# Kernel optimization log

Measured on AMD Instinct MI355X. Metric: run time of the kernel, lower is better.

## Reference

```python
import jax, jax.numpy as jnp
import numpy as np

NEG_SLOPE = 0.2

def _leaky(x):
    return jnp.where(x >= 0, x, NEG_SLOPE * x)

def _unigat(X, W, b, ae, av, pair_e, pair_v, num_v, num_e):
    # theta
    Xp = X @ W + b                                                    # [N, d]
    # v2e mean aggregation -> hyperedge features
    deg_e = jax.ops.segment_sum(jnp.ones(pair_e.shape, jnp.float32), pair_e, num_segments=num_e)
    Y = jax.ops.segment_sum(Xp[pair_v], pair_e, num_segments=num_e) / jnp.maximum(deg_e, 1.0)[:, None]  # [E, d]
    # GAT-style attention per incidence pair (edge term + node term), dropout=identity in eval
    s = _leaky((Y @ ae)[pair_e] + (Xp @ av)[pair_v])                  # [P]
    # segment softmax over edges incident to each node
    m = jax.ops.segment_max(s, pair_v, num_segments=num_v)
    ex = jnp.exp(s - m[pair_v])
    den = jax.ops.segment_sum(ex, pair_v, num_segments=num_v)
    alpha = ex / den[pair_v]                                          # [P]
    out = jax.ops.segment_sum(alpha[:, None] * Y[pair_e], pair_v, num_segments=num_v)  # [N, d]
    return jax.nn.elu(out)  # is_last=False everywhere -> ELU (use_bn=False)

def _multi_head(X, W, b, ae, av, pair_e, pair_v, num_v, num_e):
    # W:[H,din,d] b:[H,d] ae/av:[H,d]; concat heads on feature dim
    f = lambda Wh, bh, aeh, avh: _unigat(X, Wh, bh, aeh, avh, pair_e, pair_v, num_v, num_e)
    outs = jax.vmap(f)(W, b, ae, av)                                  # [H, N, d]
    return jnp.transpose(outs, (1, 0, 2)).reshape(X.shape[0], -1)     # [N, H*d]

def setup_inputs() -> dict:
    key = jax.random.key(0)
    ks = jax.random.split(key, 12)
    N, E, P = 100000, 20000, 1600000
    din, dh, H, C = 128, 64, 4, 40
    concat = 2
    inp = {
        "x0": jax.random.normal(ks[0], (N, din), jnp.float32),
        "x1": jax.random.normal(ks[1], (N, din), jnp.float32),
        "W1": jax.random.normal(ks[2], (H, din, dh), jnp.float32) * 0.05,
        "b1": jnp.zeros((H, dh), jnp.float32),
        "ae1": jax.random.normal(ks[3], (H, dh), jnp.float32) * 0.05,
        "av1": jax.random.normal(ks[4], (H, dh), jnp.float32) * 0.05,
        "W2": jax.random.normal(ks[5], (concat * dh * H, C), jnp.float32) * 0.05,
        "b2": jnp.zeros((C,), jnp.float32),
        "ae2": jax.random.normal(ks[6], (C,), jnp.float32) * 0.05,
        "av2": jax.random.normal(ks[7], (C,), jnp.float32) * 0.05,
        "pair_e": jax.random.randint(ks[8], (P,), 0, E, jnp.int32),
        "pair_v": jax.random.randint(ks[9], (P,), 0, N, jnp.int32),
        "num_v": N,
        "num_e": E,
    }
    return inp

def reference(x0, x1, W1, b1, ae1, av1, W2, b2, ae2, av2, pair_e, pair_v, num_v, num_e):
    # dropout layers are identity in eval mode
    h0 = _multi_head(x0, W1, b1, ae1, av1, pair_e, pair_v, num_v, num_e)
    h1 = _multi_head(x1, W1, b1, ae1, av1, pair_e, pair_v, num_v, num_e)
    h = jnp.concatenate([h0, h1], axis=-1)                            # [N, concat*H*dh]
    return _unigat(h, W2, b2, ae2, av2, pair_e, pair_v, num_v, num_e) # [N, C]
```

## Files before the change

### kernel.cpp

```cpp
#include <hip/hip_runtime.h>
#include <cstdint>
#include <cstddef>

static constexpr int DIN = 128;
static constexpr int DH = 64;
static constexpr int NH = 4;
static constexpr int DCAT = 512;
static constexpr int NC = 40;
static constexpr int E_CONST = 20000;
static constexpr int SH_V = 9, SUBD_V = 512;
static constexpr int SH_E = 7, SUBD_E = 128;
static constexpr int ECH = 11, NSUB_E = 10;
static constexpr int VCH = 12, NSUB_V = 25;
static constexpr int CHUNKA = 4096;

typedef unsigned short u16;
typedef __attribute__((ext_vector_type(4))) unsigned short u16x4;
typedef __attribute__((ext_vector_type(8))) unsigned short u16x8;
typedef __attribute__((ext_vector_type(8))) short bf16x8;
typedef __attribute__((ext_vector_type(4))) float f32x4;

static __device__ __forceinline__ float bf2f(u16 u) {
    union { unsigned int i; float f; } x;
    x.i = ((unsigned int)u) << 16;
    return x.f;
}
static __device__ __forceinline__ u16 f2bf(float f) {
    union { float f; unsigned int i; } x;
    x.f = f;
    unsigned int r = x.i + 0x7fffu + ((x.i >> 16) & 1u);
    return (u16)(r >> 16);
}


__global__ void k_hist2(const int* __restrict__ pv, const int* __restrict__ pe,
                        int* __restrict__ btot_v, int* __restrict__ btot_e, int P) {
    __shared__ int cv[256], ce[256];
    int tid = threadIdx.x;
    cv[tid] = 0; ce[tid] = 0;
    __syncthreads();
    int p0 = blockIdx.x * CHUNKA;
    #pragma unroll
    for (int j = 0; j < CHUNKA / 256; ++j) {
        int p = p0 + tid + j * 256;
        if (p < P) {
            atomicAdd(&cv[pv[p] >> SH_V], 1);
            atomicAdd(&ce[pe[p] >> SH_E], 1);
        }
    }
    __syncthreads();
    if (cv[tid]) atomicAdd(&btot_v[tid], cv[tid]);
    if (ce[tid]) atomicAdd(&btot_e[tid], ce[tid]);
}

static __device__ void scan_body(int* a, int n) {
    __shared__ int wsum[16];
    __shared__ int carry_s;
    int tid = threadIdx.x;
    int lane = tid & 63;
    int w = tid >> 6;
    if (tid == 0) carry_s = 0;
    __syncthreads();
    for (int base = 0; base < n; base += 1024) {
        int i = base + tid;
        int v = (i < n) ? a[i] : 0;
        int x = v;
        #pragma unroll
        for (int off = 1; off < 64; off <<= 1) {
            int t = __shfl_up(x, off);
            if (lane >= off) x += t;
        }
        if (lane == 63) wsum[w] = x;
        __syncthreads();
        int woff = 0;
        for (int k = 0; k < w; ++k) woff += wsum[k];
        int carry = carry_s;
        if (i < n) a[i] = carry + woff + x - v;
        int tot = 0;
        for (int k = 0; k < 16; ++k) tot += wsum[k];
        __syncthreads();
        if (tid == 0) carry_s = carry + tot;
        __syncthreads();
    }
    if (tid == 0) a[n] = carry_s;
}

__global__ void k_scan_both(int* __restrict__ a, int na, int* __restrict__ b, int nb) {
    if (blockIdx.x == 0) scan_body(a, na);
    else scan_body(b, nb);
}

__global__ void k_scatter2way(const int* __restrict__ pv, const int* __restrict__ pe,
                              const int* __restrict__ bstart_v, const int* __restrict__ bstart_e,
                              int* __restrict__ cur_v, int* __restrict__ cur_e,
                              uint2* __restrict__ sorted_v, uint2* __restrict__ sorted_e, int P) {
    __shared__ int cv[256], ce[256], posv[256], pose[256];
    int tid = threadIdx.x;
    cv[tid] = 0; ce[tid] = 0;
    __syncthreads();
    int p0 = blockIdx.x * CHUNKA;
    int kv[CHUNKA / 256], ke[CHUNKA / 256];
    #pragma unroll
    for (int j = 0; j < CHUNKA / 256; ++j) {
        int p = p0 + tid + j * 256;
        if (p < P) {
            kv[j] = pv[p];
            ke[j] = pe[p];
            atomicAdd(&cv[kv[j] >> SH_V], 1);
            atomicAdd(&ce[ke[j] >> SH_E], 1);
        } else {
            kv[j] = -1;
            ke[j] = -1;
        }
    }
    __syncthreads();
    if (cv[tid]) posv[tid] = bstart_v[tid] + atomicAdd(&cur_v[tid], cv[tid]);
    if (ce[tid]) pose[tid] = bstart_e[tid] + atomicAdd(&cur_e[tid], ce[tid]);
    __syncthreads();
    #pragma unroll
    for (int j = 0; j < CHUNKA / 256; ++j) {
        if (kv[j] >= 0) {
            int iv = atomicAdd(&posv[kv[j] >> SH_V], 1);
            sorted_v[iv] = make_uint2((unsigned)kv[j], (unsigned)ke[j]);
            int ie = atomicAdd(&pose[ke[j] >> SH_E], 1);
            sorted_e[ie] = make_uint2((unsigned)ke[j], (unsigned)kv[j]);
        }
    }
}

template <int SUBD, int SH, int NSUB, int CSH>
__global__ __launch_bounds__(256) void k_build_ord(const uint2* __restrict__ sorted,
                                                   const int* __restrict__ bstart,
                                                   int* __restrict__ start_out,
                                                   int* __restrict__ deg_out,
                                                   int* __restrict__ csr_out, int D) {
    constexpr int NK2 = SUBD * NSUB;
    constexpr int STRIP = (NK2 + 255) / 256;
    __shared__ int cnt[NK2];
    __shared__ int wsum[4];
    int b = blockIdx.x;
    int tid = threadIdx.x;
    int base_key = b << SH;
    int s0 = bstart[b];
    int cntN = bstart[b + 1] - s0;
    for (int k = tid; k < NK2; k += 256) cnt[k] = 0;
    __syncthreads();
    for (int i = tid; i < cntN; i += 256) {
        uint2 pr = sorted[s0 + i];
        int k2 = ((int)pr.x - base_key) * NSUB + ((int)pr.y >> CSH);
        atomicAdd(&cnt[k2], 1);
    }
    __syncthreads();
    int local[STRIP];
    int sum = 0;
    int t0 = tid * STRIP;
    #pragma unroll
    for (int j = 0; j < STRIP; ++j) {
        int idx = t0 + j;
        local[j] = (idx < NK2) ? cnt[idx] : 0;
        sum += local[j];
    }
    int lane = tid & 63, w = tid >> 6;
    int x = sum;
    #pragma unroll
    for (int off = 1; off < 64; off <<= 1) {
        int t = __shfl_up(x, off);
        if (lane >= off) x += t;
    }
    if (lane == 63) wsum[w] = x;
    __syncthreads();
    int woff = 0;
    for (int k = 0; k < w; ++k) woff += wsum[k];
    int run = woff + x - sum;
    __syncthreads();
    #pragma unroll
    for (int j = 0; j < STRIP; ++j) {
        int idx = t0 + j;
        if (idx < NK2) {
            int tmp = local[j];
            cnt[idx] = run;
            run += tmp;
        }
    }
    __syncthreads();
    for (int loc = tid; loc < SUBD; loc += 256) {
        int key = base_key + loc;
        if (key < D) {
            int st = cnt[loc * NSUB];
            int en = (loc == SUBD - 1) ? cntN : cnt[(loc + 1) * NSUB];
            start_out[key] = s0 + st;
            deg_out[key] = en - st;
        }
    }
    __syncthreads();
    for (int i = tid; i < cntN; i += 256) {
        uint2 pr = sorted[s0 + i];
        int k2 = ((int)pr.x - base_key) * NSUB + ((int)pr.y >> CSH);
        int idx = atomicAdd(&cnt[k2], 1);
        csr_out[s0 + idx] = (int)pr.y;
    }
}

__global__ void k_prep(const float* __restrict__ W1, const float* __restrict__ b1,
                       const float* __restrict__ av1, const float* __restrict__ W2,
                       float* __restrict__ wav, float* __restrict__ bav,
                       u16* __restrict__ WcatT, u16* __restrict__ W2T) {
    int bid = blockIdx.x;
    int tid = threadIdx.x;
    if (bid < 4) {
        int h = bid;
        if (tid < DIN) {
            float s = 0.f;
            for (int j = 0; j < DH; ++j)
                s += W1[(size_t)(h * DIN + tid) * DH + j] * av1[h * DH + j];
            wav[h * DIN + tid] = s;
        }
        if (tid == 0) {
            float t = 0.f;
            for (int j = 0; j < DH; ++j) t += b1[h * DH + j] * av1[h * DH + j];
            bav[h] = t;
        }
    } else if (bid < 4 + 128) {
        int idx = (bid - 4) * 256 + tid;
        int c = idx >> 7, k = idx & 127;
        int h = c >> 6, j = c & 63;
        WcatT[c * DIN + k] = f2bf(W1[((size_t)h * DIN + k) * DH + j]);
    } else {
        int idx = (bid - 132) * 256 + tid;
        int c = idx >> 9, k = idx & 511;
        float v = (c < NC) ? W2[(size_t)k * NC + c] : 0.f;
        W2T[c * DCAT + k] = f2bf(v);
    }
}

__global__ void k_conv(const float* __restrict__ X0, const float* __restrict__ X1,
                       const float* __restrict__ wav, const float* __restrict__ bav,
                       u16* __restrict__ Xbi, float* __restrict__ sv8, int N) {
    int wave = (blockIdx.x * blockDim.x + threadIdx.x) >> 6;
    int lane = threadIdx.x & 63;
    if (wave >= N) return;
    int xz = blockIdx.y;
    const float* X = xz ? X1 : X0;
    float2 a = *(const float2*)(X + (size_t)wave * DIN + lane * 2);
    unsigned int packed = (unsigned int)f2bf(a.x) | ((unsigned int)f2bf(a.y) << 16);
    *(unsigned int*)(Xbi + (size_t)wave * 256 + xz * 128 + lane * 2) = packed;
    float s[NH];
    #pragma unroll
    for (int h = 0; h < NH; ++h) {
        float2 wv = *(const float2*)(wav + h * DIN + lane * 2);
        float t = a.x * wv.x + a.y * wv.y;
        #pragma unroll
        for (int off = 32; off >= 1; off >>= 1) t += __shfl_xor(t, off);
        s[h] = t;
    }
    if (lane == 0) {
        #pragma unroll
        for (int h = 0; h < NH; ++h) sv8[(size_t)(xz * 4 + h) * N + wave] = s[h] + bav[h];
    }
}

__global__ void k_edge_mean1(const u16* __restrict__ Xbi, const int* __restrict__ start_e,
                             const int* __restrict__ deg_e, const int* __restrict__ csr_e_v,
                             u16* __restrict__ Xbar0, u16* __restrict__ Xbar1, int E) {
    int wave = (blockIdx.x * blockDim.x + threadIdx.x) >> 6;
    int lane = threadIdx.x & 63;
    if (wave >= E) return;
    int s = start_e[wave], t = s + deg_e[wave];
    int q = lane >> 4, c = lane & 15;
    float a0[8], a1[8];
    #pragma unroll
    for (int j = 0; j < 8; ++j) { a0[j] = 0.f; a1[j] = 0.f; }
    int i = s + q;
    u16x8 y0A = {0}, y1A = {0}, y0B = {0}, y1B = {0}, y0C = {0}, y1C = {0};
#define EM1_LOAD(Y0, Y1, IDX) { int v_ = csr_e_v[IDX]; \
        const u16* yp_ = Xbi + (size_t)v_ * 256 + c * 8; \
        Y0 = *(const u16x8*)yp_; Y1 = *(const u16x8*)(yp_ + 128); }
#define EM1_CONSUME(Y0, Y1) { \
        _Pragma("unroll") \
        for (int j = 0; j < 8; ++j) { a0[j] += bf2f(Y0[j]); a1[j] += bf2f(Y1[j]); } }
    if (i < t) EM1_LOAD(y0A, y1A, i);
    if (i + 4 < t) EM1_LOAD(y0B, y1B, i + 4);
    if (i + 8 < t) EM1_LOAD(y0C, y1C, i + 8);
    for (; i + 8 < t; i += 12) {
        EM1_CONSUME(y0A, y1A);
        if (i + 12 < t) EM1_LOAD(y0A, y1A, i + 12);
        EM1_CONSUME(y0B, y1B);
        if (i + 16 < t) EM1_LOAD(y0B, y1B, i + 16);
        EM1_CONSUME(y0C, y1C);
        if (i + 20 < t) EM1_LOAD(y0C, y1C, i + 20);
    }
    if (i < t) EM1_CONSUME(y0A, y1A);
    if (i + 4 < t) EM1_CONSUME(y0B, y1B);
#undef EM1_LOAD
#undef EM1_CONSUME
    #pragma unroll
    for (int j = 0; j < 8; ++j) {
        a0[j] += __shfl_xor(a0[j], 16);
        a0[j] += __shfl_xor(a0[j], 32);
        a1[j] += __shfl_xor(a1[j], 16);
        a1[j] += __shfl_xor(a1[j], 32);
    }
    int deg = t - s;
    float inv = 1.f / (float)(deg > 1 ? deg : 1);
    if (q == 0) {
        u16x8 r0, r1;
        #pragma unroll
        for (int j = 0; j < 8; ++j) { r0[j] = f2bf(a0[j] * inv); r1[j] = f2bf(a1[j] * inv); }
        *(u16x8*)(Xbar0 + (size_t)wave * DIN + c * 8) = r0;
        *(u16x8*)(Xbar1 + (size_t)wave * DIN + c * 8) = r1;
    }
}

template <int KDIM, int NTILES, int DOTMODE>
__global__ __launch_bounds__(256) void k_gemm_mfma(const u16* __restrict__ A0,
                                                   const u16* __restrict__ A1, int M,
                                                   const u16* __restrict__ Bt,
                                                   const float* __restrict__ bias,
                                                   u16* __restrict__ out0, u16* __restrict__ out1,
                                                   int ldo, int ncols,
                                                   const float* __restrict__ dvec,
                                                   float* __restrict__ dout) {
    constexpr int LDB = KDIM + 8;
    __shared__ u16 Bs[NTILES * 16 * LDB];
    const u16* A = blockIdx.z ? A1 : A0;
    u16* out = blockIdx.z ? out1 : out0;
    int tid = threadIdx.x;
    int colbase = blockIdx.y * NTILES * 16;
    const u16* Btblk = Bt + (size_t)colbase * KDIM;
    for (int idx = tid * 4; idx < NTILES * 16 * KDIM; idx += 256 * 4) {
        int c = idx / KDIM, k = idx % KDIM;
        *(u16x4*)&Bs[c * LDB + k] = *(const u16x4*)(Btblk + c * KDIM + k);
    }
    __syncthreads();
    int w = tid >> 6, lane = tid & 63;
    int r0 = blockIdx.x * 64 + w * 16;
    int arow = r0 + (lane & 15);
    bool avalid = arow < M;
    const u16* ap = A + (size_t)arow * KDIM + (lane >> 4) * 8;
    f32x4 acc[NTILES];
    #pragma unroll
    for (int nt = 0; nt < NTILES; ++nt) acc[nt] = (f32x4){0.f, 0.f, 0.f, 0.f};
    #pragma unroll
    for (int k0 = 0; k0 < KDIM; k0 += 32) {
        bf16x8 a = (bf16x8)(short)0;
        if (avalid) a = *(const bf16x8*)(ap + k0);
        #pragma unroll
        for (int nt = 0; nt < NTILES; ++nt) {
            bf16x8 b = *(const bf16x8*)&Bs[(nt * 16 + (lane & 15)) * LDB + k0 + (lane >> 4) * 8];
            acc[nt] = __builtin_amdgcn_mfma_f32_16x16x32_bf16(a, b, acc[nt], 0, 0, 0);
        }
    }
    #pragma unroll
    for (int j = 0; j < 4; ++j) {
        int row = r0 + (lane >> 4) * 4 + j;
        float pA = 0.f, pB = 0.f;
        #pragma unroll
        for (int nt = 0; nt < NTILES; ++nt) {
            int col = colbase + nt * 16 + (lane & 15);
            bool cok = col < ncols;
            float val = cok ? acc[nt][j] + bias[col] : 0.f;
            if (DOTMODE == 1) {
                float dv = dvec[col];
                if (nt < NTILES / 2) pA += val * dv; else pB += val * dv;
            } else if (DOTMODE == 2) {
                pA += cok ? val * dvec[col] : 0.f;
            }
            if (row < M && cok) out[(size_t)row * ldo + col] = f2bf(val);
        }
        if (DOTMODE) {
            pA += __shfl_xor(pA, 1);
            pA += __shfl_xor(pA, 2);
            pA += __shfl_xor(pA, 4);
            pA += __shfl_xor(pA, 8);
            if (DOTMODE == 1) {
                pB += __shfl_xor(pB, 1);
                pB += __shfl_xor(pB, 2);
                pB += __shfl_xor(pB, 4);
                pB += __shfl_xor(pB, 8);
            }
            if ((lane & 15) == 0 && row < M) {
                if (DOTMODE == 1) {
                    int hbase = blockIdx.y * 2;
                    int z = blockIdx.z;
                    dout[(size_t)(z * 4 + hbase) * M + row] = pA;
                    dout[(size_t)(z * 4 + hbase + 1) * M + row] = pB;
                } else {
                    dout[row] = pA;
                }
            }
        }
    }
}

__global__ void k_node_pass1(const u16* __restrict__ Ycat, const float* __restrict__ se8,
                             const float* __restrict__ sv8, const int* __restrict__ start_v,
                             const int* __restrict__ deg_v, const int* __restrict__ csr_v_e,
                             u16* __restrict__ hbuf, int N, int E) {
    int bid = blockIdx.x;
    int s = bid & 7;
    int warp = threadIdx.x >> 6;
    int lane = threadIdx.x & 63;
    int g = lane >> 3, c = lane & 7;
    int node = (bid >> 3) * 32 + warp * 8 + g;
    if (node >= N) return;
    int p0 = start_v[node];
    int p1 = p0 + deg_v[node];
    float sv = sv8[(size_t)s * N + node];
    const float* seS = se8 + (size_t)s * E;
    const u16* ybase = Ycat + s * 64 + c * 8;
    float den = 0.f;
    float acc[8];
    #pragma unroll
    for (int j = 0; j < 8; ++j) acc[j] = 0.f;
    float sA = 0.f, sB = 0.f;
    u16x8 yA = {0}, yB = {0};
#define NP1_LOAD(S, Y, IDX) { int e_ = csr_v_e[IDX]; S = seS[e_]; \
        Y = *(const u16x8*)(ybase + (size_t)e_ * 512); }
#define NP1_CONSUME(S, Y) { \
        float x_ = S + sv; x_ = fmaxf(x_, 0.2f * x_); float ex_ = __expf(x_); \
        den += ex_; \
        _Pragma("unroll") \
        for (int j = 0; j < 8; ++j) acc[j] += ex_ * bf2f(Y[j]); }
    int i = p0;
    if (i < p1) NP1_LOAD(sA, yA, i);
    if (i + 1 < p1) NP1_LOAD(sB, yB, i + 1);
    for (; i + 1 < p1; i += 2) {
        NP1_CONSUME(sA, yA);
        if (i + 2 < p1) NP1_LOAD(sA, yA, i + 2);
        NP1_CONSUME(sB, yB);
        if (i + 3 < p1) NP1_LOAD(sB, yB, i + 3);
    }
    if (i < p1) NP1_CONSUME(sA, yA);
#undef NP1_LOAD
#undef NP1_CONSUME
    float inv = (p1 > p0) ? 1.f / den : 0.f;
    u16x8 r;
    #pragma unroll
    for (int j = 0; j < 8; ++j) {
        float o = acc[j] * inv;
        o = o > 0.f ? o : __expf(o) - 1.f;
        r[j] = f2bf(o);
    }
    *(u16x8*)(hbuf + (size_t)node * DCAT + s * 64 + c * 8) = r;
}


__global__ void k_edge_mean2(const u16* __restrict__ Xp2b, const int* __restrict__ start_e,
                             const int* __restrict__ deg_ea, const int* __restrict__ csr_e_v,
                             u16* __restrict__ Y2b, const float* __restrict__ ae2,
                             float* __restrict__ se2, int E) {
    int warp = threadIdx.x >> 6;
    int lane = threadIdx.x & 63;
    int g = lane >> 3, c = lane & 7;
    int edge = blockIdx.x * 32 + warp * 8 + g;
    if (edge >= E) return;
    int p0 = start_e[edge], p1 = p0 + deg_ea[edge];
    bool act = c < 5;
    const u16* xbase = Xp2b + c * 8;
    float acc[8];
    #pragma unroll
    for (int j = 0; j < 8; ++j) acc[j] = 0.f;
    if (act) {
        for (int i = p0; i < p1; ++i) {
            int v = csr_e_v[i];
            u16x8 y = *(const u16x8*)(xbase + (size_t)v * NC);
            #pragma unroll
            for (int j = 0; j < 8; ++j) acc[j] += bf2f(y[j]);
        }
    }
    int deg = p1 - p0;
    float inv = 1.f / (float)(deg > 1 ? deg : 1);
    float p = 0.f;
    if (act) {
        u16x8 r;
        #pragma unroll
        for (int j = 0; j < 8; ++j) {
            float y = acc[j] * inv;
            p += y * ae2[c * 8 + j];
            r[j] = f2bf(y);
        }
        *(u16x8*)(Y2b + (size_t)edge * NC + c * 8) = r;
    }
    p += __shfl_xor(p, 1);
    p += __shfl_xor(p, 2);
    p += __shfl_xor(p, 4);
    if (c == 0) se2[edge] = p;
}

__global__ void k_node_pass2(const u16* __restrict__ Y2b, const float* __restrict__ se2,
                             const float* __restrict__ sv2, const int* __restrict__ start_v,
                             const int* __restrict__ deg_va, const int* __restrict__ csr_v_e,
                             float* __restrict__ out, int N) {
    int warp = threadIdx.x >> 6;
    int lane = threadIdx.x & 63;
    int g = lane >> 3, c = lane & 7;
    int node = blockIdx.x * 32 + warp * 8 + g;
    if (node >= N) return;
    int p0 = start_v[node], p1 = p0 + deg_va[node];
    bool act = c < 5;
    float* orow = out + (size_t)node * NC;
    if (p1 == p0) {
        if (act) {
            *(float4*)(orow + c * 8) = make_float4(0.f, 0.f, 0.f, 0.f);
            *(float4*)(orow + c * 8 + 4) = make_float4(0.f, 0.f, 0.f, 0.f);
        }
        return;
    }
    float svv = sv2[node];
    const u16* ybase = Y2b + c * 8;
    float den = 0.f;
    float acc[8];
    #pragma unroll
    for (int j = 0; j < 8; ++j) acc[j] = 0.f;
    for (int i = p0; i < p1; ++i) {
        int e = csr_v_e[i];
        float x = se2[e] + svv;
        x = fmaxf(x, 0.2f * x);
        float ex = __expf(x);
        den += ex;
        if (act) {
            u16x8 y = *(const u16x8*)(ybase + (size_t)e * NC);
            #pragma unroll
            for (int j = 0; j < 8; ++j) acc[j] += ex * bf2f(y[j]);
        }
    }
    if (act) {
        float inv = 1.f / den;
        float o[8];
        #pragma unroll
        for (int j = 0; j < 8; ++j) {
            float v = acc[j] * inv;
            o[j] = v > 0.f ? v : __expf(v) - 1.f;
        }
        *(float4*)(orow + c * 8) = make_float4(o[0], o[1], o[2], o[3]);
        *(float4*)(orow + c * 8 + 4) = make_float4(o[4], o[5], o[6], o[7]);
    }
}

extern "C" void kernel_launch(void* const* d_in, const int* in_sizes, int n_in,
                              void* d_out, int out_size, void* d_ws, size_t ws_size,
                              hipStream_t stream) {
    const float* x0 = (const float*)d_in[0];
    const float* x1 = (const float*)d_in[1];
    const float* W1 = (const float*)d_in[2];
    const float* b1 = (const float*)d_in[3];
    const float* ae1 = (const float*)d_in[4];
    const float* av1 = (const float*)d_in[5];
    const float* W2 = (const float*)d_in[6];
    const float* b2 = (const float*)d_in[7];
    const float* ae2 = (const float*)d_in[8];
    const float* av2 = (const float*)d_in[9];
    const int* pe = (const int*)d_in[10];
    const int* pv = (const int*)d_in[11];

    const int N = in_sizes[0] / DIN;
    const int P = in_sizes[10];
    const int E = E_CONST;
    const int NBKT_V = (N + SUBD_V - 1) / SUBD_V;
    const int NBKT_E = (E + SUBD_E - 1) / SUBD_E;

    char* base = (char*)d_ws;
    auto alloc = [&](size_t bytes) -> void* {
        void* p = (void*)base;
        base += (bytes + 255) & ~(size_t)255;
        return p;
    };
    u16* Xbi = (u16*)alloc((size_t)N * 256 * 2);
    u16* hbuf = (u16*)alloc((size_t)N * DCAT * 2);
    u16* Xbar0 = (u16*)alloc((size_t)E * DIN * 2);
    u16* Xbar1 = (u16*)alloc((size_t)E * DIN * 2);
    u16* Ycat = (u16*)alloc((size_t)E * 512 * 2);
    u16* Xp2b = (u16*)alloc((size_t)N * NC * 2);
    u16* Y2b = (u16*)alloc((size_t)E * NC * 2);
    float* se8 = (float*)alloc((size_t)8 * E * 4);
    float* se2 = (float*)alloc((size_t)E * 4);
    float* sv8 = (float*)alloc((size_t)8 * N * 4);
    float* sv2 = (float*)alloc((size_t)N * 4);
    float* wav = (float*)alloc((size_t)NH * DIN * 4);
    float* bav = (float*)alloc((size_t)NH * 4);
    u16* WcatT = (u16*)alloc((size_t)256 * DIN * 2);
    u16* W2T = (u16*)alloc((size_t)48 * DCAT * 2);
    uint2* sorted_v = (uint2*)alloc((size_t)P * 8);
    uint2* sorted_e = (uint2*)alloc((size_t)P * 8);
    int* start_v = (int*)alloc((size_t)N * 4);
    int* deg_v = (int*)alloc((size_t)N * 4);
    int* start_e = (int*)alloc((size_t)E * 4);
    int* deg_e = (int*)alloc((size_t)E * 4);
    int* csr_v_e = (int*)alloc((size_t)P * 4);
    int* csr_e_v = (int*)alloc((size_t)P * 4);
    char* zstart = base;
    int* bstart_v = (int*)alloc((size_t)(NBKT_V + 1) * 4);
    int* bstart_e = (int*)alloc((size_t)(NBKT_E + 1) * 4);
    int* cur_v = (int*)alloc((size_t)256 * 4);
    int* cur_e = (int*)alloc((size_t)256 * 4);
    size_t zbytes = (size_t)(base - zstart);

    if ((size_t)(base - (char*)d_ws) > ws_size) return;

    hipMemsetAsync(zstart, 0, zbytes, stream);

    dim3 b256(256);
    int nA = (P + CHUNKA - 1) / CHUNKA;
    k_hist2<<<nA, b256, 0, stream>>>(pv, pe, bstart_v, bstart_e, P);
    k_scan_both<<<2, 1024, 0, stream>>>(bstart_v, NBKT_V, bstart_e, NBKT_E);
    k_scatter2way<<<nA, b256, 0, stream>>>(pv, pe, bstart_v, bstart_e, cur_v, cur_e,
                                           sorted_v, sorted_e, P);
    k_build_ord<SUBD_V, SH_V, NSUB_E, ECH><<<NBKT_V, b256, 0, stream>>>(sorted_v, bstart_v,
                                                                        start_v, deg_v,
                                                                        csr_v_e, N);
    k_build_ord<SUBD_E, SH_E, NSUB_V, VCH><<<NBKT_E, b256, 0, stream>>>(sorted_e, bstart_e,
                                                                        start_e, deg_e,
                                                                        csr_e_v, E);

    k_prep<<<228, b256, 0, stream>>>(W1, b1, av1, W2, wav, bav, WcatT, W2T);

    int gN4 = (N + 3) / 4;
    int gE4 = (E + 3) / 4;
    dim3 gconv(gN4, 2);
    k_conv<<<gconv, b256, 0, stream>>>(x0, x1, wav, bav, Xbi, sv8, N);

    k_edge_mean1<<<gE4, b256, 0, stream>>>(Xbi, start_e, deg_e, csr_e_v, Xbar0, Xbar1, E);
    dim3 g1((E + 63) / 64, 2, 2);
    k_gemm_mfma<DIN, 8, 1><<<g1, b256, 0, stream>>>(Xbar0, Xbar1, E, WcatT, b1,
                                                    Ycat, Ycat + 256, 512, 256, ae1, se8);
    int gnp1 = ((N + 31) / 32) * 8;
    k_node_pass1<<<gnp1, b256, 0, stream>>>(Ycat, se8, sv8, start_v, deg_v, csr_v_e,
                                            hbuf, N, E);

    dim3 g2((N + 63) / 64, 1, 1);
    k_gemm_mfma<DCAT, 3, 2><<<g2, b256, 0, stream>>>(hbuf, hbuf, N, W2T, b2, Xp2b, Xp2b,
                                                     NC, NC, av2, sv2);
    int gseg = (E + 31) / 32;
    k_edge_mean2<<<gseg, b256, 0, stream>>>(Xp2b, start_e, deg_e, csr_e_v, Y2b, ae2, se2, E);
    int gnp2 = (N + 31) / 32;
    k_node_pass2<<<gnp2, b256, 0, stream>>>(Y2b, se2, sv2, start_v, deg_v, csr_v_e,
                                            (float*)d_out, N);
}
```

Baseline: 600.5 us.

## Process nodes and edges in degree-sorted order to balance warp work

Adds a counting sort of nodes and hyperedges by degree that builds a permutation, and makes node_pass1, edge_mean2 and node_pass2 visit items in that order. The goal is that the eight groups within a warp see similar segment lengths, so fewer lanes sit idle waiting on the longest segment. In exchange it adds five small launches for the sort plus one extra indirection per item, and output writes become scattered rather than contiguous.

Result: slower. 677.0 us (+12.7%).

```diff
diff --git a/kernel.cpp b/kernel.cpp
--- a/kernel.cpp
+++ b/kernel.cpp
@@ -13,6 +13,7 @@
 static constexpr int ECH = 11, NSUB_E = 10;
 static constexpr int VCH = 12, NSUB_V = 25;
 static constexpr int CHUNKA = 4096;
+static constexpr int DCH = 2048;
 
 typedef unsigned short u16;
 typedef __attribute__((ext_vector_type(4))) unsigned short u16x4;
@@ -198,6 +199,48 @@
         int k2 = ((int)pr.x - base_key) * NSUB + ((int)pr.y >> CSH);
         int idx = atomicAdd(&cnt[k2], 1);
         csr_out[s0 + idx] = (int)pr.y;
+    }
+}
+
+
+__global__ void k_deg_hist(const int* __restrict__ deg, int n, int* __restrict__ btot) {
+    __shared__ int h[1024];
+    int tid = threadIdx.x;
+    for (int k = tid; k < 1024; k += 256) h[k] = 0;
+    __syncthreads();
+    int base = blockIdx.x * DCH;
+    int end = base + DCH < n ? base + DCH : n;
+    for (int i = base + tid; i < end; i += 256) {
+        int d = deg[i];
+        atomicAdd(&h[d < 1023 ? d : 1023], 1);
+    }
+    __syncthreads();
+    for (int k = tid; k < 1024; k += 256)
+        if (h[k]) atomicAdd(&btot[k], h[k]);
+}
+
+__global__ void k_deg_scatter(const int* __restrict__ deg, int n,
+                              const int* __restrict__ bstart, int* __restrict__ cur,
+                              int* __restrict__ perm) {
+    __shared__ int h[1024], pos[1024];
+    int tid = threadIdx.x;
+    for (int k = tid; k < 1024; k += 256) h[k] = 0;
+    __syncthreads();
+    int base = blockIdx.x * DCH;
+    int end = base + DCH < n ? base + DCH : n;
+    for (int i = base + tid; i < end; i += 256) {
+        int d = deg[i];
+        atomicAdd(&h[d < 1023 ? d : 1023], 1);
+    }
+    __syncthreads();
+    for (int k = tid; k < 1024; k += 256)
+        if (h[k]) pos[k] = bstart[k] + atomicAdd(&cur[k], h[k]);
+    __syncthreads();
+    for (int i = base + tid; i < end; i += 256) {
+        int d = deg[i];
+        int b = d < 1023 ? d : 1023;
+        int p = atomicAdd(&pos[b], 1);
+        perm[p] = i;
     }
 }
 
@@ -395,14 +438,16 @@
 __global__ void k_node_pass1(const u16* __restrict__ Ycat, const float* __restrict__ se8,
                              const float* __restrict__ sv8, const int* __restrict__ start_v,
                              const int* __restrict__ deg_v, const int* __restrict__ csr_v_e,
-                             u16* __restrict__ hbuf, int N, int E) {
+                             const int* __restrict__ perm, u16* __restrict__ hbuf,
+                             int N, int E) {
     int bid = blockIdx.x;
     int s = bid & 7;
     int warp = threadIdx.x >> 6;
     int lane = threadIdx.x & 63;
     int g = lane >> 3, c = lane & 7;
-    int node = (bid >> 3) * 32 + warp * 8 + g;
-    if (node >= N) return;
+    int gidx = (bid >> 3) * 32 + warp * 8 + g;
+    if (gidx >= N) return;
+    int node = perm[gidx];
     int p0 = start_v[node];
     int p1 = p0 + deg_v[node];
     float sv = sv8[(size_t)s * N + node];
@@ -447,13 +492,14 @@
 
 __global__ void k_edge_mean2(const u16* __restrict__ Xp2b, const int* __restrict__ start_e,
                              const int* __restrict__ deg_ea, const int* __restrict__ csr_e_v,
-                             u16* __restrict__ Y2b, const float* __restrict__ ae2,
-                             float* __restrict__ se2, int E) {
+                             const int* __restrict__ perm, u16* __restrict__ Y2b,
+                             const float* __restrict__ ae2, float* __restrict__ se2, int E) {
     int warp = threadIdx.x >> 6;
     int lane = threadIdx.x & 63;
     int g = lane >> 3, c = lane & 7;
-    int edge = blockIdx.x * 32 + warp * 8 + g;
-    if (edge >= E) return;
+    int gidx = blockIdx.x * 32 + warp * 8 + g;
+    if (gidx >= E) return;
+    int edge = perm[gidx];
     int p0 = start_e[edge], p1 = p0 + deg_ea[edge];
     bool act = c < 5;
     const u16* xbase = Xp2b + c * 8;
@@ -490,12 +536,13 @@
 __global__ void k_node_pass2(const u16* __restrict__ Y2b, const float* __restrict__ se2,
                              const float* __restrict__ sv2, const int* __restrict__ start_v,
                              const int* __restrict__ deg_va, const int* __restrict__ csr_v_e,
-                             float* __restrict__ out, int N) {
+                             const int* __restrict__ perm, float* __restrict__ out, int N) {
     int warp = threadIdx.x >> 6;
     int lane = threadIdx.x & 63;
     int g = lane >> 3, c = lane & 7;
-    int node = blockIdx.x * 32 + warp * 8 + g;
-    if (node >= N) return;
+    int gidx = blockIdx.x * 32 + warp * 8 + g;
+    if (gidx >= N) return;
+    int node = perm[gidx];
     int p0 = start_v[node], p1 = p0 + deg_va[node];
     bool act = c < 5;
     float* orow = out + (size_t)node * NC;
@@ -588,11 +635,17 @@
     int* deg_e = (int*)alloc((size_t)E * 4);
     int* csr_v_e = (int*)alloc((size_t)P * 4);
     int* csr_e_v = (int*)alloc((size_t)P * 4);
+    int* perm_v = (int*)alloc((size_t)N * 4);
+    int* perm_e = (int*)alloc((size_t)E * 4);
     char* zstart = base;
     int* bstart_v = (int*)alloc((size_t)(NBKT_V + 1) * 4);
     int* bstart_e = (int*)alloc((size_t)(NBKT_E + 1) * 4);
     int* cur_v = (int*)alloc((size_t)256 * 4);
     int* cur_e = (int*)alloc((size_t)256 * 4);
+    int* dhist_v = (int*)alloc((size_t)1025 * 4);
+    int* dhist_e = (int*)alloc((size_t)1025 * 4);
+    int* dcur_v = (int*)alloc((size_t)1024 * 4);
+    int* dcur_e = (int*)alloc((size_t)1024 * 4);
     size_t zbytes = (size_t)(base - zstart);
 
     if ((size_t)(base - (char*)d_ws) > ws_size) return;
@@ -612,6 +665,14 @@
                                                                         start_e, deg_e,
                                                                         csr_e_v, E);
 
+    int nDV = (N + DCH - 1) / DCH;
+    int nDE = (E + DCH - 1) / DCH;
+    k_deg_hist<<<nDV, b256, 0, stream>>>(deg_v, N, dhist_v);
+    k_deg_hist<<<nDE, b256, 0, stream>>>(deg_e, E, dhist_e);
+    k_scan_both<<<2, 1024, 0, stream>>>(dhist_v, 1024, dhist_e, 1024);
+    k_deg_scatter<<<nDV, b256, 0, stream>>>(deg_v, N, dhist_v, dcur_v, perm_v);
+    k_deg_scatter<<<nDE, b256, 0, stream>>>(deg_e, E, dhist_e, dcur_e, perm_e);
+
     k_prep<<<228, b256, 0, stream>>>(W1, b1, av1, W2, wav, bav, WcatT, W2T);
 
     int gN4 = (N + 3) / 4;
@@ -625,14 +686,15 @@
                                                     Ycat, Ycat + 256, 512, 256, ae1, se8);
     int gnp1 = ((N + 31) / 32) * 8;
     k_node_pass1<<<gnp1, b256, 0, stream>>>(Ycat, se8, sv8, start_v, deg_v, csr_v_e,
-                                            hbuf, N, E);
+                                            perm_v, hbuf, N, E);
 
     dim3 g2((N + 63) / 64, 1, 1);
     k_gemm_mfma<DCAT, 3, 2><<<g2, b256, 0, stream>>>(hbuf, hbuf, N, W2T, b2, Xp2b, Xp2b,
                                                      NC, NC, av2, sv2);
     int gseg = (E + 31) / 32;
-    k_edge_mean2<<<gseg, b256, 0, stream>>>(Xp2b, start_e, deg_e, csr_e_v, Y2b, ae2, se2, E);
+    k_edge_mean2<<<gseg, b256, 0, stream>>>(Xp2b, start_e, deg_e, csr_e_v, perm_e,
+                                            Y2b, ae2, se2, E);
     int gnp2 = (N + 31) / 32;
     k_node_pass2<<<gnp2, b256, 0, stream>>>(Y2b, se2, sv2, start_v, deg_v, csr_v_e,
-                                            (float*)d_out, N);
-}
+                                            perm_v, (float*)d_out, N);
+}
```
